# Optimization experiments

Hardware: AMD Instinct MI355X
Metric: run time of the kernel (lower is better)

## Reference

```python
import jax, jax.numpy as jnp
import numpy as np

# Paul Kellet pink-noise filter coefficients (verbatim from the torch source)
_A = np.array([0.99886, 0.99332, 0.969, 0.8665, 0.55, -0.7616], dtype=np.float32)   # pole feedback
_C = np.array([0.0555179, 0.0750759, 0.153852, 0.3104856, 0.5329522, -0.016898], dtype=np.float32)  # input gains
_B6_GAIN = 0.115926   # b6 is the previous white sample scaled (one-sample delay)
_DIRECT = 0.5362      # direct white feedthrough
_OUT_GAIN = 0.11


def setup_inputs() -> dict:
    key = jax.random.key(0)
    B, L = 256, 65536
    white = jax.random.normal(key, (B, L), dtype=jnp.float32)
    return {"white": white}


def reference(white):
    """Pink noise via the 6-pole IIR recurrence from SignalGenerator.noise('pink'),
    vectorized over a batch of channels; sequential time handled by lax.scan.
    white: [B, L] -> pink: [B, L]
    """
    B, L = white.shape
    a = jnp.asarray(_A)  # [6]
    c = jnp.asarray(_C)  # [6]

    def step(carry, w_t):
        # carry: (b [B,6] pole states, b6 [B] delayed-white state); w_t: [B]
        b, b6 = carry
        b = a * b + w_t[:, None] * c                      # [B,6]
        pink_t = (b.sum(-1) + b6 + _DIRECT * w_t) * _OUT_GAIN  # [B]
        return (b, _B6_GAIN * w_t), pink_t

    init = (jnp.zeros((B, 6), dtype=white.dtype), jnp.zeros((B,), dtype=white.dtype))
    _, pink_tb = jax.lax.scan(step, init, white.T)  # scan over time: [L, B]
    return pink_tb.T  # [B, L]
```

## Files before the change

kernel.cpp:

```cpp
#include <hip/hip_runtime.h>


constexpr int kL = 65536;
constexpr int kThreads = 512;
constexpr int kWaves = kThreads / 64;
constexpr int kStage = 8192;
constexpr int kStages = kL / kStage;
constexpr int kChunk = kStage / kThreads;
constexpr int kF4 = kStage / 4 / kThreads;

__device__ __forceinline__ int swz(int i) {
    return i ^ (((i >> 5) & 7) << 2);
}

__device__ __forceinline__ void wg_barrier() {
    asm volatile("s_waitcnt lgkmcnt(0)" ::: "memory");
    __builtin_amdgcn_s_barrier();
    asm volatile("" ::: "memory");
}

__global__ __launch_bounds__(kThreads) void pink_kernel(
    const float* __restrict__ white, float* __restrict__ pink)
{
    constexpr float A[6] = {0.99886f, 0.99332f, 0.969f, 0.8665f, 0.55f, -0.7616f};
    constexpr float C[6] = {0.0555179f, 0.0750759f, 0.153852f, 0.3104856f, 0.5329522f, -0.016898f};
    constexpr float B6G = 0.115926f, DIRECT = 0.5362f, OUTG = 0.11f;

    __shared__ __align__(16) float buf[2][kStage];

    const int tid = threadIdx.x, lane = tid & 63, wave = tid >> 6;
    const float* __restrict__ wrow = white + (size_t)blockIdx.x * kL;
    float*       __restrict__ prow = pink  + (size_t)blockIdx.x * kL;

    float m16[6], Mwv[6], Mst[6], pmL[6], pmW[6];
    #pragma unroll
    for (int p = 0; p < 6; ++p) {
        float q = A[p];
        #pragma unroll
        for (int i = 0; i < 4; ++i) q *= q;
        m16[p] = q;
        float pm = 1.f, qq = q;
        #pragma unroll
        for (int b = 0; b < 6; ++b) { if ((lane >> b) & 1) pm *= qq; qq *= qq; }
        pmL[p] = pm;
        float mw = q;
        #pragma unroll
        for (int i = 0; i < 6; ++i) mw *= mw;
        Mwv[p] = mw;
        float pv = 1.f, qw = mw;
        #pragma unroll
        for (int b = 0; b < 3; ++b) { if ((wave >> b) & 1) pv *= qw; qw *= qw; }
        pmW[p] = pv;
        Mst[p] = qw;
    }

    float S[6];
    #pragma unroll
    for (int p = 0; p < 6; ++p) S[p] = 0.f;

    float4 nxt[kF4];
    {
        const float4* src = (const float4*)wrow;
        #pragma unroll
        for (int k = 0; k < kF4; ++k) nxt[k] = src[tid + k * kThreads];
        #pragma unroll
        for (int k = 0; k < kF4; ++k)
            *(float4*)&buf[0][swz(4 * (tid + k * kThreads))] = nxt[k];
    }

    for (int s = 0; s < kStages; ++s) {
        const int cur = s & 1, nb = cur ^ 1;

        if (s > 0) {
            float4 o[kF4];
            #pragma unroll
            for (int k = 0; k < kF4; ++k)
                o[k] = *(const float4*)&buf[nb][swz(4 * (tid + k * kThreads))];
            float4* dst = (float4*)(prow + (size_t)(s - 1) * kStage);
            #pragma unroll
            for (int k = 0; k < kF4; ++k) dst[tid + k * kThreads] = o[k];
        }
        if (s + 1 < kStages) {
            const float4* src = (const float4*)(wrow + (size_t)(s + 1) * kStage);
            #pragma unroll
            for (int k = 0; k < kF4; ++k) nxt[k] = src[tid + k * kThreads];
        }
        wg_barrier();

        float w[kChunk];
        #pragma unroll
        for (int kk = 0; kk < kChunk / 4; ++kk) {
            float4 v = *(const float4*)&buf[cur][swz(kChunk * tid + 4 * kk)];
            w[4*kk] = v.x; w[4*kk+1] = v.y; w[4*kk+2] = v.z; w[4*kk+3] = v.w;
        }
        float pw;
        if (tid == 0) pw = (s == 0) ? 0.f : wrow[(size_t)s * kStage - 1];
        else          pw = buf[cur][swz(kChunk * tid - 1)];

        float e[6];
        #pragma unroll
        for (int p = 0; p < 6; ++p) e[p] = 0.f;
        #pragma unroll
        for (int k = 0; k < kChunk; ++k) {
            const float ww = w[k];
            #pragma unroll
            for (int p = 0; p < 6; ++p) e[p] = fmaf(A[p], e[p], ww * C[p]);
        }

        float mk[6];
        #pragma unroll
        for (int p = 0; p < 6; ++p) mk[p] = m16[p];
        #pragma unroll
        for (int r = 0; r < 6; ++r) {
            const int off = 1 << r;
            float fe[6];
            #pragma unroll
            for (int p = 0; p < 6; ++p) fe[p] = __shfl_up(e[p], off);
            if (lane >= off) {
                #pragma unroll
                for (int p = 0; p < 6; ++p) e[p] = fmaf(mk[p], fe[p], e[p]);
            }
            #pragma unroll
            for (int p = 0; p < 6; ++p) mk[p] *= mk[p];
        }
        float ex[6];
        #pragma unroll
        for (int p = 0; p < 6; ++p) {
            ex[p] = __shfl_up(e[p], 1);
            if (lane == 0) ex[p] = 0.f;
        }

        float* seb = &buf[nb][0];
        if (lane == 63) {
            #pragma unroll
            for (int p = 0; p < 6; ++p) seb[p * 8 + wave] = e[p];
        }
        wg_barrier();

        float P[6], Etot[6];
        #pragma unroll
        for (int p = 0; p < 6; ++p) {
            float4 lo = *(const float4*)&seb[p * 8];
            float4 hi = *(const float4*)&seb[p * 8 + 4];
            const float sv[8] = {lo.x, lo.y, lo.z, lo.w, hi.x, hi.y, hi.z, hi.w};
            float Pp = 0.f, Ep = 0.f;
            #pragma unroll
            for (int w2 = 0; w2 < kWaves; ++w2) {
                if (w2 < wave) Pp = fmaf(Mwv[p], Pp, sv[w2]);
                Ep = fmaf(Mwv[p], Ep, sv[w2]);
            }
            P[p] = Pp; Etot[p] = Ep;
        }

        float b[6];
        #pragma unroll
        for (int p = 0; p < 6; ++p) {
            const float PS = fmaf(pmW[p], S[p], P[p]);
            b[p] = fmaf(pmL[p], PS, ex[p]);
            S[p] = fmaf(Mst[p], S[p], Etot[p]);
        }
        float b6 = B6G * pw;

        wg_barrier();

        #pragma unroll
        for (int kk = 0; kk < kChunk / 4; ++kk) {
            float4 o;
            float* op = &o.x;
            #pragma unroll
            for (int j = 0; j < 4; ++j) {
                const float ww = w[4*kk + j];
                #pragma unroll
                for (int p = 0; p < 6; ++p) b[p] = fmaf(A[p], b[p], ww * C[p]);
                const float sum = ((b[0]+b[1]) + (b[2]+b[3])) + ((b[4]+b[5]) + b6);
                op[j] = fmaf(DIRECT, ww, sum) * OUTG;
                b6 = B6G * ww;
            }
            *(float4*)&buf[cur][swz(kChunk * tid + 4 * kk)] = o;
        }

        if (s + 1 < kStages) {
            #pragma unroll
            for (int k = 0; k < kF4; ++k)
                *(float4*)&buf[nb][swz(4 * (tid + k * kThreads))] = nxt[k];
        }
        wg_barrier();
    }

    {
        const int lastb = (kStages - 1) & 1;
        float4* dst = (float4*)(prow + (size_t)(kStages - 1) * kStage);
        #pragma unroll
        for (int k = 0; k < kF4; ++k) {
            float4 o = *(const float4*)&buf[lastb][swz(4 * (tid + k * kThreads))];
            dst[tid + k * kThreads] = o;
        }
    }
}

extern "C" void kernel_launch(void* const* d_in, const int* in_sizes, int n_in,
                              void* d_out, int out_size, void* d_ws, size_t ws_size,
                              hipStream_t stream) {
    const float* white = (const float*)d_in[0];
    float* pink = (float*)d_out;
    const int B = in_sizes[0] / kL;
    hipLaunchKernelGGL(pink_kernel, dim3(B), dim3(kThreads), 0, stream,
                       white, pink);
}
```

Baseline: 151.8 us.

## Split pink-noise scan into tile totals, tile prefix, and output kernels

Replaces the single one-block-per-channel sequential-stage kernel with a three-pass scan. Pass one computes each 4096-sample tile's decayed state contribution, pass two does a short sequential prefix over 16 tiles per channel, and pass three recomputes each tile's outputs from its carried-in state. This spreads work across 4096 blocks instead of 256 so more of the GPU is busy. The cost is reading the input twice and launching two extra kernels.

```diff
diff --git a/kernel.cpp b/kernel.cpp
--- a/kernel.cpp
+++ b/kernel.cpp
@@ -2,37 +2,135 @@
 
 
 constexpr int kL = 65536;
-constexpr int kThreads = 512;
-constexpr int kWaves = kThreads / 64;
-constexpr int kStage = 8192;
-constexpr int kStages = kL / kStage;
-constexpr int kChunk = kStage / kThreads;
-constexpr int kF4 = kStage / 4 / kThreads;
+constexpr int kTile = 4096;
+constexpr int kThr = 256;
+constexpr int kChunk = 16;
+constexpr int kTilesPerCh = kL / kTile;
 
 __device__ __forceinline__ int swz(int i) {
     return i ^ (((i >> 5) & 7) << 2);
 }
 
-__device__ __forceinline__ void wg_barrier() {
-    asm volatile("s_waitcnt lgkmcnt(0)" ::: "memory");
-    __builtin_amdgcn_s_barrier();
-    asm volatile("" ::: "memory");
-}
-
-__global__ __launch_bounds__(kThreads) void pink_kernel(
-    const float* __restrict__ white, float* __restrict__ pink)
+__global__ __launch_bounds__(kThr) void pink_tile_totals(
+    const float* __restrict__ white, float* __restrict__ tile_e, int nTiles)
+{
+    constexpr float A[6] = {0.99886f, 0.99332f, 0.969f, 0.8665f, 0.55f, -0.7616f};
+    constexpr float C[6] = {0.0555179f, 0.0750759f, 0.153852f, 0.3104856f, 0.5329522f, -0.016898f};
+
+    __shared__ __align__(16) float buf[kTile];
+    __shared__ float ssum[6][4];
+
+    const int tid = threadIdx.x, lane = tid & 63, wave = tid >> 6;
+    const int blk = blockIdx.x;
+
+    const float4* src = (const float4*)(white + (size_t)blk * kTile);
+    float4 v[4];
+    #pragma unroll
+    for (int k = 0; k < 4; ++k) v[k] = src[tid + k * kThr];
+    #pragma unroll
+    for (int k = 0; k < 4; ++k)
+        *(float4*)&buf[swz(4 * (tid + k * kThr))] = v[k];
+
+    float pmR[6];
+    #pragma unroll
+    for (int p = 0; p < 6; ++p) {
+        float q = A[p];
+        #pragma unroll
+        for (int i = 0; i < 4; ++i) q *= q;
+        float pm = 1.f;
+        const int r = 255 - tid;
+        #pragma unroll
+        for (int b = 0; b < 8; ++b) { if ((r >> b) & 1) pm *= q; q *= q; }
+        pmR[p] = pm;
+    }
+    __syncthreads();
+
+    float w[kChunk];
+    #pragma unroll
+    for (int kk = 0; kk < kChunk / 4; ++kk) {
+        float4 x = *(const float4*)&buf[swz(kChunk * tid + 4 * kk)];
+        w[4*kk] = x.x; w[4*kk+1] = x.y; w[4*kk+2] = x.z; w[4*kk+3] = x.w;
+    }
+
+    float e[6] = {0.f, 0.f, 0.f, 0.f, 0.f, 0.f};
+    #pragma unroll
+    for (int k = 0; k < kChunk; ++k) {
+        const float ww = w[k];
+        #pragma unroll
+        for (int p = 0; p < 6; ++p) e[p] = fmaf(A[p], e[p], ww * C[p]);
+    }
+    #pragma unroll
+    for (int p = 0; p < 6; ++p) e[p] *= pmR[p];
+
+    #pragma unroll
+    for (int m = 1; m < 64; m <<= 1) {
+        #pragma unroll
+        for (int p = 0; p < 6; ++p) e[p] += __shfl_xor(e[p], m);
+    }
+    if (lane == 0) {
+        #pragma unroll
+        for (int p = 0; p < 6; ++p) ssum[p][wave] = e[p];
+    }
+    __syncthreads();
+    if (tid < 6)
+        tile_e[(size_t)tid * nTiles + blk] =
+            ssum[tid][0] + ssum[tid][1] + ssum[tid][2] + ssum[tid][3];
+}
+
+__global__ __launch_bounds__(256) void pink_tile_prefix(
+    const float* __restrict__ tile_e, float* __restrict__ tile_P, int nTiles)
+{
+    constexpr float A[6] = {0.99886f, 0.99332f, 0.969f, 0.8665f, 0.55f, -0.7616f};
+    const int p  = blockIdx.x;
+    const int ch = blockIdx.y * 256 + threadIdx.x;
+    const int nCh = nTiles / kTilesPerCh;
+    if (ch >= nCh) return;
+
+    float Mt = A[p];
+    #pragma unroll
+    for (int i = 0; i < 12; ++i) Mt *= Mt;
+
+    const float* ep = tile_e + (size_t)p * nTiles + (size_t)ch * kTilesPerCh;
+    float*       Pp = tile_P + (size_t)p * nTiles + (size_t)ch * kTilesPerCh;
+    float P = 0.f;
+    #pragma unroll
+    for (int t = 0; t < kTilesPerCh; ++t) {
+        Pp[t] = P;
+        P = fmaf(Mt, P, ep[t]);
+    }
+}
+
+__global__ __launch_bounds__(kThr) void pink_outputs(
+    const float* __restrict__ white, const float* __restrict__ tile_P,
+    float* __restrict__ pink, int nTiles)
 {
     constexpr float A[6] = {0.99886f, 0.99332f, 0.969f, 0.8665f, 0.55f, -0.7616f};
     constexpr float C[6] = {0.0555179f, 0.0750759f, 0.153852f, 0.3104856f, 0.5329522f, -0.016898f};
     constexpr float B6G = 0.115926f, DIRECT = 0.5362f, OUTG = 0.11f;
 
-    __shared__ __align__(16) float buf[2][kStage];
+    __shared__ __align__(16) float buf[kTile];
+    __shared__ float swv[6][4];
 
     const int tid = threadIdx.x, lane = tid & 63, wave = tid >> 6;
-    const float* __restrict__ wrow = white + (size_t)blockIdx.x * kL;
-    float*       __restrict__ prow = pink  + (size_t)blockIdx.x * kL;
-
-    float m16[6], Mwv[6], Mst[6], pmL[6], pmW[6];
+    const int blk = blockIdx.x;
+    const size_t base = (size_t)blk * kTile;
+
+    float P[6];
+    #pragma unroll
+    for (int p = 0; p < 6; ++p) P[p] = tile_P[(size_t)p * nTiles + blk];
+
+    float pw0 = 0.f;
+    if (tid == 0 && (blk & (kTilesPerCh - 1)) != 0) pw0 = white[base - 1];
+
+    const float4* src = (const float4*)(white + base);
+    float4 v[4];
+    #pragma unroll
+    for (int k = 0; k < 4; ++k) v[k] = src[tid + k * kThr];
+    #pragma unroll
+    for (int k = 0; k < 4; ++k)
+        *(float4*)&buf[swz(4 * (tid + k * kThr))] = v[k];
+
+    float m16[6], pmL[6], Mwv[6];
     #pragma unroll
     for (int p = 0; p < 6; ++p) {
         float q = A[p];
@@ -43,159 +141,86 @@
         #pragma unroll
         for (int b = 0; b < 6; ++b) { if ((lane >> b) & 1) pm *= qq; qq *= qq; }
         pmL[p] = pm;
-        float mw = q;
-        #pragma unroll
-        for (int i = 0; i < 6; ++i) mw *= mw;
-        Mwv[p] = mw;
-        float pv = 1.f, qw = mw;
-        #pragma unroll
-        for (int b = 0; b < 3; ++b) { if ((wave >> b) & 1) pv *= qw; qw *= qw; }
-        pmW[p] = pv;
-        Mst[p] = qw;
-    }
-
-    float S[6];
-    #pragma unroll
-    for (int p = 0; p < 6; ++p) S[p] = 0.f;
-
-    float4 nxt[kF4];
-    {
-        const float4* src = (const float4*)wrow;
-        #pragma unroll
-        for (int k = 0; k < kF4; ++k) nxt[k] = src[tid + k * kThreads];
-        #pragma unroll
-        for (int k = 0; k < kF4; ++k)
-            *(float4*)&buf[0][swz(4 * (tid + k * kThreads))] = nxt[k];
-    }
-
-    for (int s = 0; s < kStages; ++s) {
-        const int cur = s & 1, nb = cur ^ 1;
-
-        if (s > 0) {
-            float4 o[kF4];
+        Mwv[p] = qq;
+    }
+    __syncthreads();
+
+    float w[kChunk];
+    #pragma unroll
+    for (int kk = 0; kk < kChunk / 4; ++kk) {
+        float4 x = *(const float4*)&buf[swz(kChunk * tid + 4 * kk)];
+        w[4*kk] = x.x; w[4*kk+1] = x.y; w[4*kk+2] = x.z; w[4*kk+3] = x.w;
+    }
+    const float pwl = (tid == 0) ? pw0 : buf[swz(kChunk * tid - 1)];
+
+    float e[6] = {0.f, 0.f, 0.f, 0.f, 0.f, 0.f};
+    #pragma unroll
+    for (int k = 0; k < kChunk; ++k) {
+        const float ww = w[k];
+        #pragma unroll
+        for (int p = 0; p < 6; ++p) e[p] = fmaf(A[p], e[p], ww * C[p]);
+    }
+
+    float mk[6];
+    #pragma unroll
+    for (int p = 0; p < 6; ++p) mk[p] = m16[p];
+    #pragma unroll
+    for (int r = 0; r < 6; ++r) {
+        const int off = 1 << r;
+        float fe[6];
+        #pragma unroll
+        for (int p = 0; p < 6; ++p) fe[p] = __shfl_up(e[p], off);
+        if (lane >= off) {
             #pragma unroll
-            for (int k = 0; k < kF4; ++k)
-                o[k] = *(const float4*)&buf[nb][swz(4 * (tid + k * kThreads))];
-            float4* dst = (float4*)(prow + (size_t)(s - 1) * kStage);
+            for (int p = 0; p < 6; ++p) e[p] = fmaf(mk[p], fe[p], e[p]);
+        }
+        #pragma unroll
+        for (int p = 0; p < 6; ++p) mk[p] *= mk[p];
+    }
+    float ex[6];
+    #pragma unroll
+    for (int p = 0; p < 6; ++p) {
+        ex[p] = __shfl_up(e[p], 1);
+        if (lane == 0) ex[p] = 0.f;
+    }
+    if (lane == 63) {
+        #pragma unroll
+        for (int p = 0; p < 6; ++p) swv[p][wave] = e[p];
+    }
+    __syncthreads();
+
+    float b[6];
+    #pragma unroll
+    for (int p = 0; p < 6; ++p) {
+        float X = P[p];
+        #pragma unroll
+        for (int w2 = 0; w2 < 3; ++w2)
+            if (w2 < wave) X = fmaf(Mwv[p], X, swv[p][w2]);
+        b[p] = fmaf(pmL[p], X, ex[p]);
+    }
+    float b6 = B6G * pwl;
+
+    #pragma unroll
+    for (int kk = 0; kk < kChunk / 4; ++kk) {
+        float4 o;
+        float* op = &o.x;
+        #pragma unroll
+        for (int j = 0; j < 4; ++j) {
+            const float ww = w[4*kk + j];
             #pragma unroll
-            for (int k = 0; k < kF4; ++k) dst[tid + k * kThreads] = o[k];
+            for (int p = 0; p < 6; ++p) b[p] = fmaf(A[p], b[p], ww * C[p]);
+            const float sum = ((b[0]+b[1]) + (b[2]+b[3])) + ((b[4]+b[5]) + b6);
+            op[j] = fmaf(DIRECT, ww, sum) * OUTG;
+            b6 = B6G * ww;
         }
-        if (s + 1 < kStages) {
-            const float4* src = (const float4*)(wrow + (size_t)(s + 1) * kStage);
-            #pragma unroll
-            for (int k = 0; k < kF4; ++k) nxt[k] = src[tid + k * kThreads];
-        }
-        wg_barrier();
-
-        float w[kChunk];
-        #pragma unroll
-        for (int kk = 0; kk < kChunk / 4; ++kk) {
-            float4 v = *(const float4*)&buf[cur][swz(kChunk * tid + 4 * kk)];
-            w[4*kk] = v.x; w[4*kk+1] = v.y; w[4*kk+2] = v.z; w[4*kk+3] = v.w;
-        }
-        float pw;
-        if (tid == 0) pw = (s == 0) ? 0.f : wrow[(size_t)s * kStage - 1];
-        else          pw = buf[cur][swz(kChunk * tid - 1)];
-
-        float e[6];
-        #pragma unroll
-        for (int p = 0; p < 6; ++p) e[p] = 0.f;
-        #pragma unroll
-        for (int k = 0; k < kChunk; ++k) {
-            const float ww = w[k];
-            #pragma unroll
-            for (int p = 0; p < 6; ++p) e[p] = fmaf(A[p], e[p], ww * C[p]);
-        }
-
-        float mk[6];
-        #pragma unroll
-        for (int p = 0; p < 6; ++p) mk[p] = m16[p];
-        #pragma unroll
-        for (int r = 0; r < 6; ++r) {
-            const int off = 1 << r;
-            float fe[6];
-            #pragma unroll
-            for (int p = 0; p < 6; ++p) fe[p] = __shfl_up(e[p], off);
-            if (lane >= off) {
-                #pragma unroll
-                for (int p = 0; p < 6; ++p) e[p] = fmaf(mk[p], fe[p], e[p]);
-            }
-            #pragma unroll
-            for (int p = 0; p < 6; ++p) mk[p] *= mk[p];
-        }
-        float ex[6];
-        #pragma unroll
-        for (int p = 0; p < 6; ++p) {
-            ex[p] = __shfl_up(e[p], 1);
-            if (lane == 0) ex[p] = 0.f;
-        }
-
-        float* seb = &buf[nb][0];
-        if (lane == 63) {
-            #pragma unroll
-            for (int p = 0; p < 6; ++p) seb[p * 8 + wave] = e[p];
-        }
-        wg_barrier();
-
-        float P[6], Etot[6];
-        #pragma unroll
-        for (int p = 0; p < 6; ++p) {
-            float4 lo = *(const float4*)&seb[p * 8];
-            float4 hi = *(const float4*)&seb[p * 8 + 4];
-            const float sv[8] = {lo.x, lo.y, lo.z, lo.w, hi.x, hi.y, hi.z, hi.w};
-            float Pp = 0.f, Ep = 0.f;
-            #pragma unroll
-            for (int w2 = 0; w2 < kWaves; ++w2) {
-                if (w2 < wave) Pp = fmaf(Mwv[p], Pp, sv[w2]);
-                Ep = fmaf(Mwv[p], Ep, sv[w2]);
-            }
-            P[p] = Pp; Etot[p] = Ep;
-        }
-
-        float b[6];
-        #pragma unroll
-        for (int p = 0; p < 6; ++p) {
-            const float PS = fmaf(pmW[p], S[p], P[p]);
-            b[p] = fmaf(pmL[p], PS, ex[p]);
-            S[p] = fmaf(Mst[p], S[p], Etot[p]);
-        }
-        float b6 = B6G * pw;
-
-        wg_barrier();
-
-        #pragma unroll
-        for (int kk = 0; kk < kChunk / 4; ++kk) {
-            float4 o;
-            float* op = &o.x;
-            #pragma unroll
-            for (int j = 0; j < 4; ++j) {
-                const float ww = w[4*kk + j];
-                #pragma unroll
-                for (int p = 0; p < 6; ++p) b[p] = fmaf(A[p], b[p], ww * C[p]);
-                const float sum = ((b[0]+b[1]) + (b[2]+b[3])) + ((b[4]+b[5]) + b6);
-                op[j] = fmaf(DIRECT, ww, sum) * OUTG;
-                b6 = B6G * ww;
-            }
-            *(float4*)&buf[cur][swz(kChunk * tid + 4 * kk)] = o;
-        }
-
-        if (s + 1 < kStages) {
-            #pragma unroll
-            for (int k = 0; k < kF4; ++k)
-                *(float4*)&buf[nb][swz(4 * (tid + k * kThreads))] = nxt[k];
-        }
-        wg_barrier();
-    }
-
-    {
-        const int lastb = (kStages - 1) & 1;
-        float4* dst = (float4*)(prow + (size_t)(kStages - 1) * kStage);
-        #pragma unroll
-        for (int k = 0; k < kF4; ++k) {
-            float4 o = *(const float4*)&buf[lastb][swz(4 * (tid + k * kThreads))];
-            dst[tid + k * kThreads] = o;
-        }
-    }
+        *(float4*)&buf[swz(kChunk * tid + 4 * kk)] = o;
+    }
+    __syncthreads();
+
+    float4* dst = (float4*)(pink + base);
+    #pragma unroll
+    for (int k = 0; k < 4; ++k)
+        dst[tid + k * kThr] = *(const float4*)&buf[swz(4 * (tid + k * kThr))];
 }
 
 extern "C" void kernel_launch(void* const* d_in, const int* in_sizes, int n_in,
@@ -203,7 +228,15 @@
                               hipStream_t stream) {
     const float* white = (const float*)d_in[0];
     float* pink = (float*)d_out;
-    const int B = in_sizes[0] / kL;
-    hipLaunchKernelGGL(pink_kernel, dim3(B), dim3(kThreads), 0, stream,
-                       white, pink);
-}
+    const int nTiles = in_sizes[0] / kTile;
+    const int nCh = nTiles / kTilesPerCh;
+    float* tile_e = (float*)d_ws;
+    float* tile_P = tile_e + (size_t)6 * nTiles;
+
+    hipLaunchKernelGGL(pink_tile_totals, dim3(nTiles), dim3(kThr), 0, stream,
+                       white, tile_e, nTiles);
+    hipLaunchKernelGGL(pink_tile_prefix, dim3(6, (nCh + 255) / 256), dim3(256),
+                       0, stream, tile_e, tile_P, nTiles);
+    hipLaunchKernelGGL(pink_outputs, dim3(nTiles), dim3(kThr), 0, stream,
+                       white, tile_P, pink, nTiles);
+}
```

New measurement: 127.3 us. 16.2% less time.
